# Kernel tuning notes

Hardware: AMD Instinct MI355X
Metric: run time of the kernel (lower is better)

Reference implementation:

```python
import jax, jax.numpy as jnp
import numpy as np

B, S, F, H = 2048, 512, 64, 256

def setup_inputs() -> dict:
    key = jax.random.key(0)
    ks = jax.random.split(key, 9)
    s = 0.05
    return {
        "x": jax.random.normal(ks[0], (B, S, F), jnp.float32),
        "h0": jax.random.normal(ks[1], (1, B, H), jnp.float32),
        "c0": jax.random.normal(ks[2], (1, B, H), jnp.float32),
        "W_ih": jax.random.normal(ks[3], (4 * H, F), jnp.float32) * s,
        "W_hh": jax.random.normal(ks[4], (4 * H, H), jnp.float32) * s,
        "b_ih": jax.random.normal(ks[5], (4 * H,), jnp.float32) * s,
        "b_hh": jax.random.normal(ks[6], (4 * H,), jnp.float32) * s,
        "W_dense": jax.random.normal(ks[7], (F, H), jnp.float32) * s,
        "b_dense": jax.random.normal(ks[8], (F,), jnp.float32) * s,
        "seq_len": S,
    }

def reference(x, h0, c0, W_ih, W_hh, b_ih, b_hh, W_dense, b_dense, seq_len):
    # h_0 tensors are [1, B, H]; original squeezes dim 0.
    h = h0[0]
    c = c0[0]
    bias = b_ih + b_hh  # [4H]
    Hd = W_hh.shape[1]

    def dense(v):  # [B, H] -> [B, F]
        return v @ W_dense.T + b_dense

    # epsilon = 0.0 => teacher forcing never used; next input is dense(c_t).
    x_t = dense(h)

    def step(carry, _):
        h, c, x_t = carry
        gates = x_t @ W_ih.T + h @ W_hh.T + bias  # [B, 4H]
        i = jax.nn.sigmoid(gates[:, 0 * Hd:1 * Hd])
        f = jax.nn.sigmoid(gates[:, 1 * Hd:2 * Hd])
        g = jnp.tanh(gates[:, 2 * Hd:3 * Hd])
        o = jax.nn.sigmoid(gates[:, 3 * Hd:4 * Hd])
        c_new = f * c + i * g
        h_new = o * jnp.tanh(c_new)
        # Original: h_t = (h', c'); x_t = dense(h_t[1]) = dense(c'); output[:, t] = dense(c')
        y = c_new @ W_dense.T + b_dense
        return (h_new, c_new, y), y

    (_, _, _), ys = jax.lax.scan(step, (h, c, x_t), None, length=seq_len)
    # ys: [S, B, F] -> [B, S, F]
    return jnp.transpose(ys, (1, 0, 2))
```

## Files before the change

kernel.cpp:

```cpp
#include <hip/hip_runtime.h>
#include <stdint.h>

#define SEQ   512
#define FD    64
#define HD    256
#define ZSTR  324
#define CSTR  260

#define GRPB      5120
#define WGB       (8 * GRPB)
#define DENSE_OFF (16 * WGB)
typedef __attribute__((ext_vector_type(8))) __bf16 bf16x8;
typedef __attribute__((ext_vector_type(4))) float  f32x4;

__device__ __forceinline__ float sigm(float x) {
    return __builtin_amdgcn_rcpf(1.0f + __expf(-x));
}
__device__ __forceinline__ float tanh_(float x) {
    return 2.0f * __builtin_amdgcn_rcpf(1.0f + __expf(-2.0f * x)) - 1.0f;
}

__global__ __launch_bounds__(64) void prep_weights(
    const float* __restrict__ W_ih, const float* __restrict__ W_hh,
    const float* __restrict__ W_dense, __bf16* __restrict__ wsb)
{
    const int b = blockIdx.x, l = threadIdx.x, lr = l & 15, lg = l >> 4;
    if (b < 128) {
        const int w = b >> 3, i = b & 7;
        const int h = (i >> 2) & 1, nt = i & 3;
        const int n = nt * 256 + w * 16 + lr;
        for (int c = 0; c < 5; ++c) {
            const int k0 = h * 160 + c * 32 + lg * 8;
            const float* src = (k0 < 64) ? (W_ih + n * 64 + k0)
                                         : (W_hh + n * 256 + (k0 - 64));
            bf16x8 v;
            for (int e = 0; e < 8; ++e) v[e] = (__bf16)src[e];
            *(bf16x8*)(wsb + (size_t)(b * 5 + c) * 512 + l * 8) = v;
        }
    } else {
        const int d = b - 128;
        const int f = d * 16 + lr;
        for (int c = 0; c < 8; ++c) {
            const float* src = W_dense + f * 256 + c * 32 + lg * 8;
            bf16x8 v;
            for (int e = 0; e < 8; ++e) v[e] = (__bf16)src[e];
            *(bf16x8*)(wsb + DENSE_OFF / 2 + d * 4096 + c * 512 + l * 8) = v;
        }
    }
}

__global__ __launch_bounds__(1024, 4) void lstm_persist(
    const float* __restrict__ h0, const float* __restrict__ c0,
    const float* __restrict__ b_ih, const float* __restrict__ b_hh,
    const float* __restrict__ b_dense, const __bf16* __restrict__ wsb,
    float* __restrict__ out)
{
    __shared__ __align__(16) __bf16 Zb[2 * 16 * ZSTR];
    __shared__ __align__(16) __bf16 CBb[16 * CSTR];

    const int tid = threadIdx.x;
    const int w   = tid >> 6;
    const int l   = tid & 63;
    const int lr  = l & 15;
    const int lg  = l >> 4;
    const int row0 = blockIdx.x * 16;
    const int jj  = w * 16 + lr;

    const __bf16* wgbase = wsb + (size_t)w * (WGB / 2);
    const __bf16* wdbase = wsb + DENSE_OFF / 2 + w * 4096 + l * 8;

    float biasv[4];
    float creg[4];
#pragma unroll
    for (int nt = 0; nt < 4; ++nt) {
        const int n = nt * 256 + jj;
        biasv[nt] = b_ih[n] + b_hh[n];
    }
#pragma unroll
    for (int r = 0; r < 4; ++r)
        creg[r] = c0[(size_t)(row0 + lg * 4 + r) * HD + jj];
    float ybias = (w < 4) ? b_dense[w * 16 + lr] : 0.0f;

    {
        const int e0 = tid * 4;
        const int m  = e0 >> 8;
        const int j4 = e0 & 255;
        const float4 hv = *(const float4*)(h0 + (size_t)(row0 + m) * HD + j4);
        __bf16* zp = &Zb[m * ZSTR + 64 + j4];
        zp[0] = (__bf16)hv.x; zp[1] = (__bf16)hv.y;
        zp[2] = (__bf16)hv.z; zp[3] = (__bf16)hv.w;
    }
    __syncthreads();

    if (w < 4) {
        f32x4 ya = {ybias, ybias, ybias, ybias};
#pragma unroll
        for (int c = 0; c < 8; ++c) {
            bf16x8 wdc = *(const bf16x8*)(wdbase + c * 512);
            bf16x8 av  = *(const bf16x8*)(&Zb[lr * ZSTR + 64 + c * 32 + lg * 8]);
            ya = __builtin_amdgcn_mfma_f32_16x16x32_bf16(av, wdc, ya, 0, 0, 0);
        }
#pragma unroll
        for (int r = 0; r < 4; ++r)
            Zb[(lg * 4 + r) * ZSTR + w * 16 + lr] = (__bf16)ya[r];
    }

    float* outp = out + (size_t)row0 * SEQ * FD;

    for (int t = 0; t < SEQ; ++t) {
        __syncthreads();

        const __bf16* Zc = Zb + (t & 1) * (16 * ZSTR);
        __bf16*       Zn = Zb + ((t + 1) & 1) * (16 * ZSTR);

        const __bf16* gp = wgbase + l * 8;
        asm volatile("" : "+v"(gp));

        bf16x8 sA[5], sB[5];
#pragma unroll
        for (int c = 0; c < 5; ++c) sA[c] = *(const bf16x8*)(gp + c * 512);
#pragma unroll
        for (int c = 0; c < 5; ++c) sB[c] = *(const bf16x8*)(gp + 2560 + c * 512);

        bf16x8 aph[5];
        f32x4  acc[4];

#pragma unroll
        for (int i = 0; i < 8; ++i) {
            const int h = i >> 2, nt = i & 3;

            if ((i & 3) == 0) {
#pragma unroll
                for (int c = 0; c < 5; ++c)
                    aph[c] = *(const bf16x8*)(&Zc[lr * ZSTR + (h * 5 + c) * 32 + lg * 8]);
            }

            const float bb = biasv[nt];
            f32x4 cc = (h == 0) ? f32x4{bb, bb, bb, bb} : acc[nt];
            if ((i & 1) == 0) {
                cc = __builtin_amdgcn_mfma_f32_16x16x32_bf16(aph[0], sA[0], cc, 0, 0, 0);
                cc = __builtin_amdgcn_mfma_f32_16x16x32_bf16(aph[1], sA[1], cc, 0, 0, 0);
                cc = __builtin_amdgcn_mfma_f32_16x16x32_bf16(aph[2], sA[2], cc, 0, 0, 0);
                cc = __builtin_amdgcn_mfma_f32_16x16x32_bf16(aph[3], sA[3], cc, 0, 0, 0);
                cc = __builtin_amdgcn_mfma_f32_16x16x32_bf16(aph[4], sA[4], cc, 0, 0, 0);
                if (i + 2 < 8) {
#pragma unroll
                    for (int c = 0; c < 5; ++c)
                        sA[c] = *(const bf16x8*)(gp + (i + 2) * 2560 + c * 512);
                }
            } else {
                cc = __builtin_amdgcn_mfma_f32_16x16x32_bf16(aph[0], sB[0], cc, 0, 0, 0);
                cc = __builtin_amdgcn_mfma_f32_16x16x32_bf16(aph[1], sB[1], cc, 0, 0, 0);
                cc = __builtin_amdgcn_mfma_f32_16x16x32_bf16(aph[2], sB[2], cc, 0, 0, 0);
                cc = __builtin_amdgcn_mfma_f32_16x16x32_bf16(aph[3], sB[3], cc, 0, 0, 0);
                cc = __builtin_amdgcn_mfma_f32_16x16x32_bf16(aph[4], sB[4], cc, 0, 0, 0);
                if (i + 2 < 8) {
#pragma unroll
                    for (int c = 0; c < 5; ++c)
                        sB[c] = *(const bf16x8*)(gp + (i + 2) * 2560 + c * 512);
                }
            }
            acc[nt] = cc;

            if (i == 7) {
#pragma unroll
                for (int r = 0; r < 4; ++r) {
                    const int m = lg * 4 + r;
                    const float ig = sigm(acc[0][r]);
                    const float fg = sigm(acc[1][r]);
                    const float gg = tanh_(acc[2][r]);
                    const float og = sigm(acc[3][r]);
                    const float cn = fg * creg[r] + ig * gg;
                    creg[r] = cn;
                    const float hn = og * tanh_(cn);
                    Zn[m * ZSTR + 64 + jj] = (__bf16)hn;
                    CBb[m * CSTR + jj]     = (__bf16)cn;
                }
            }
        }

        __syncthreads();

        if (w < 4) {
            const __bf16* wdp = wdbase;
            asm volatile("" : "+v"(wdp));
            f32x4 ya = {ybias, ybias, ybias, ybias};
#pragma unroll
            for (int c = 0; c < 8; ++c) {
                bf16x8 wdc = *(const bf16x8*)(wdp + c * 512);
                bf16x8 acb = *(const bf16x8*)(&CBb[lr * CSTR + c * 32 + lg * 8]);
                ya = __builtin_amdgcn_mfma_f32_16x16x32_bf16(acb, wdc, ya, 0, 0, 0);
            }
            const int f = w * 16 + lr;
#pragma unroll
            for (int r = 0; r < 4; ++r) {
                const int m = lg * 4 + r;
                outp[(size_t)m * (SEQ * FD) + t * FD + f] = ya[r];
                Zn[m * ZSTR + f] = (__bf16)ya[r];
            }
        }
    }
}

extern "C" void kernel_launch(void* const* d_in, const int* in_sizes, int n_in,
                              void* d_out, int out_size, void* d_ws, size_t ws_size,
                              hipStream_t stream) {
    (void)in_sizes; (void)n_in; (void)ws_size; (void)out_size;
    const float* h0      = (const float*)d_in[1];
    const float* c0      = (const float*)d_in[2];
    const float* W_ih    = (const float*)d_in[3];
    const float* W_hh    = (const float*)d_in[4];
    const float* b_ih    = (const float*)d_in[5];
    const float* b_hh    = (const float*)d_in[6];
    const float* W_dense = (const float*)d_in[7];
    const float* b_dense = (const float*)d_in[8];
    __bf16* wsb = (__bf16*)d_ws;

    prep_weights<<<132, 64, 0, stream>>>(W_ih, W_hh, W_dense, wsb);
    lstm_persist<<<128, 1024, 0, stream>>>(h0, c0, b_ih, b_hh, b_dense, wsb, (float*)d_out);
}
```

Measured before the change: 3.569 ms.

## Halve block size so each wave computes two hidden-column slices per step

Shrinks the persistent LSTM block from 16 to 8 waves, so each wave now processes two 16-column hidden slices (16 MFMA groups instead of 8) and keeps two sets of bias and cell state in registers. The weight prep layout is rearranged to match, and the h0 load is widened to 8 elements per thread. The aim is to cut barrier cost and raise per-wave work and MFMA issue density per step. The trade-off is fewer waves available to hide latency and a longer serial chain inside each wave.

Result: slower. 3.820 ms (+7.0%).

```diff
diff --git a/kernel.cpp b/kernel.cpp
--- a/kernel.cpp
+++ b/kernel.cpp
@@ -8,8 +8,9 @@
 #define CSTR  260
 
 #define GRPB      5120
-#define WGB       (8 * GRPB)
-#define DENSE_OFF (16 * WGB)
+#define WGB       (16 * GRPB)
+#define DENSE_OFF (8 * WGB)
+
 typedef __attribute__((ext_vector_type(8))) __bf16 bf16x8;
 typedef __attribute__((ext_vector_type(4))) float  f32x4;
 
@@ -26,16 +27,16 @@
 {
     const int b = blockIdx.x, l = threadIdx.x, lr = l & 15, lg = l >> 4;
     if (b < 128) {
-        const int w = b >> 3, i = b & 7;
-        const int h = (i >> 2) & 1, nt = i & 3;
-        const int n = nt * 256 + w * 16 + lr;
+        const int w = b >> 4, i = b & 15;
+        const int s = 2 * w + (i >> 3), h = (i >> 2) & 1, nt = i & 3;
+        const int n = nt * 256 + s * 16 + lr;
         for (int c = 0; c < 5; ++c) {
             const int k0 = h * 160 + c * 32 + lg * 8;
             const float* src = (k0 < 64) ? (W_ih + n * 64 + k0)
                                          : (W_hh + n * 256 + (k0 - 64));
             bf16x8 v;
             for (int e = 0; e < 8; ++e) v[e] = (__bf16)src[e];
-            *(bf16x8*)(wsb + (size_t)(b * 5 + c) * 512 + l * 8) = v;
+            *(bf16x8*)(wsb + (size_t)((w * 16 + i) * 5 + c) * 512 + l * 8) = v;
         }
     } else {
         const int d = b - 128;
@@ -49,7 +50,8 @@
     }
 }
 
-__global__ __launch_bounds__(1024, 4) void lstm_persist(
+__global__ __launch_bounds__(512) __attribute__((amdgpu_waves_per_eu(2, 2)))
+void lstm_persist(
     const float* __restrict__ h0, const float* __restrict__ c0,
     const float* __restrict__ b_ih, const float* __restrict__ b_hh,
     const float* __restrict__ b_dense, const __bf16* __restrict__ wsb,
@@ -64,31 +66,35 @@
     const int lr  = l & 15;
     const int lg  = l >> 4;
     const int row0 = blockIdx.x * 16;
-    const int jj  = w * 16 + lr;
 
     const __bf16* wgbase = wsb + (size_t)w * (WGB / 2);
     const __bf16* wdbase = wsb + DENSE_OFF / 2 + w * 4096 + l * 8;
 
-    float biasv[4];
-    float creg[4];
-#pragma unroll
-    for (int nt = 0; nt < 4; ++nt) {
-        const int n = nt * 256 + jj;
-        biasv[nt] = b_ih[n] + b_hh[n];
-    }
-#pragma unroll
-    for (int r = 0; r < 4; ++r)
-        creg[r] = c0[(size_t)(row0 + lg * 4 + r) * HD + jj];
+    float biasv[2][4];
+    float creg[2][4];
+#pragma unroll
+    for (int p = 0; p < 2; ++p) {
+        const int jj = (2 * w + p) * 16 + lr;
+#pragma unroll
+        for (int nt = 0; nt < 4; ++nt) {
+            const int n = nt * 256 + jj;
+            biasv[p][nt] = b_ih[n] + b_hh[n];
+        }
+#pragma unroll
+        for (int r = 0; r < 4; ++r)
+            creg[p][r] = c0[(size_t)(row0 + lg * 4 + r) * HD + jj];
+    }
     float ybias = (w < 4) ? b_dense[w * 16 + lr] : 0.0f;
 
     {
-        const int e0 = tid * 4;
+        const int e0 = tid * 8;
         const int m  = e0 >> 8;
-        const int j4 = e0 & 255;
-        const float4 hv = *(const float4*)(h0 + (size_t)(row0 + m) * HD + j4);
-        __bf16* zp = &Zb[m * ZSTR + 64 + j4];
-        zp[0] = (__bf16)hv.x; zp[1] = (__bf16)hv.y;
-        zp[2] = (__bf16)hv.z; zp[3] = (__bf16)hv.w;
+        const int j8 = e0 & 255;
+        const float4 h1 = *(const float4*)(h0 + (size_t)(row0 + m) * HD + j8);
+        const float4 h2 = *(const float4*)(h0 + (size_t)(row0 + m) * HD + j8 + 4);
+        __bf16* zp = &Zb[m * ZSTR + 64 + j8];
+        zp[0] = (__bf16)h1.x; zp[1] = (__bf16)h1.y; zp[2] = (__bf16)h1.z; zp[3] = (__bf16)h1.w;
+        zp[4] = (__bf16)h2.x; zp[5] = (__bf16)h2.y; zp[6] = (__bf16)h2.z; zp[7] = (__bf16)h2.w;
     }
     __syncthreads();
 
@@ -126,8 +132,8 @@
         f32x4  acc[4];
 
 #pragma unroll
-        for (int i = 0; i < 8; ++i) {
-            const int h = i >> 2, nt = i & 3;
+        for (int i = 0; i < 16; ++i) {
+            const int p = i >> 3, h = (i >> 2) & 1, nt = i & 3;
 
             if ((i & 3) == 0) {
 #pragma unroll
@@ -135,7 +141,7 @@
                     aph[c] = *(const bf16x8*)(&Zc[lr * ZSTR + (h * 5 + c) * 32 + lg * 8]);
             }
 
-            const float bb = biasv[nt];
+            const float bb = biasv[p][nt];
             f32x4 cc = (h == 0) ? f32x4{bb, bb, bb, bb} : acc[nt];
             if ((i & 1) == 0) {
                 cc = __builtin_amdgcn_mfma_f32_16x16x32_bf16(aph[0], sA[0], cc, 0, 0, 0);
@@ -143,7 +149,7 @@
                 cc = __builtin_amdgcn_mfma_f32_16x16x32_bf16(aph[2], sA[2], cc, 0, 0, 0);
                 cc = __builtin_amdgcn_mfma_f32_16x16x32_bf16(aph[3], sA[3], cc, 0, 0, 0);
                 cc = __builtin_amdgcn_mfma_f32_16x16x32_bf16(aph[4], sA[4], cc, 0, 0, 0);
-                if (i + 2 < 8) {
+                if (i + 2 < 16) {
 #pragma unroll
                     for (int c = 0; c < 5; ++c)
                         sA[c] = *(const bf16x8*)(gp + (i + 2) * 2560 + c * 512);
@@ -154,7 +160,7 @@
                 cc = __builtin_amdgcn_mfma_f32_16x16x32_bf16(aph[2], sB[2], cc, 0, 0, 0);
                 cc = __builtin_amdgcn_mfma_f32_16x16x32_bf16(aph[3], sB[3], cc, 0, 0, 0);
                 cc = __builtin_amdgcn_mfma_f32_16x16x32_bf16(aph[4], sB[4], cc, 0, 0, 0);
-                if (i + 2 < 8) {
+                if (i + 2 < 16) {
 #pragma unroll
                     for (int c = 0; c < 5; ++c)
                         sB[c] = *(const bf16x8*)(gp + (i + 2) * 2560 + c * 512);
@@ -162,7 +168,8 @@
             }
             acc[nt] = cc;
 
-            if (i == 7) {
+            if ((i & 7) == 7) {
+                const int jj = (2 * w + p) * 16 + lr;
 #pragma unroll
                 for (int r = 0; r < 4; ++r) {
                     const int m = lg * 4 + r;
@@ -170,8 +177,8 @@
                     const float fg = sigm(acc[1][r]);
                     const float gg = tanh_(acc[2][r]);
                     const float og = sigm(acc[3][r]);
-                    const float cn = fg * creg[r] + ig * gg;
-                    creg[r] = cn;
+                    const float cn = fg * creg[p][r] + ig * gg;
+                    creg[p][r] = cn;
                     const float hn = og * tanh_(cn);
                     Zn[m * ZSTR + 64 + jj] = (__bf16)hn;
                     CBb[m * CSTR + jj]     = (__bf16)cn;
@@ -217,5 +224,5 @@
     __bf16* wsb = (__bf16*)d_ws;
 
     prep_weights<<<132, 64, 0, stream>>>(W_ih, W_hh, W_dense, wsb);
-    lstm_persist<<<128, 1024, 0, stream>>>(h0, c0, b_ih, b_hh, b_dense, wsb, (float*)d_out);
-}
+    lstm_persist<<<128, 512, 0, stream>>>(h0, c0, b_ih, b_hh, b_dense, wsb, (float*)d_out);
+}
```
